# Performance work log

Measured on AMD Instinct MI355X. Metric: run time of the kernel, lower is better.

The kernel has to match this reference:

```python
import jax, jax.numpy as jnp
import numpy as np


def setup_inputs() -> dict:
    key = jax.random.key(0)
    kq, kk, kv = jax.random.split(key, 3)
    B, H, S, D = 4, 16, 2048, 64
    q = jax.random.normal(kq, (B, H, S, D), dtype=jnp.float32)
    k = jax.random.normal(kk, (B, H, S, D), dtype=jnp.float32)
    v = jax.random.normal(kv, (B, H, S, D), dtype=jnp.float32)
    return {"q": q, "k": k, "v": v}


def reference(q, k, v):
    # Flash-attention math (causal=True, softmax_scale = 1/sqrt(head_dim)).
    D = q.shape[-1]
    scale = 1.0 / np.sqrt(D).astype(np.float32)
    # scores: [B, H, Sq, Sk]
    scores = jnp.einsum('bhqd,bhkd->bhqk', q, k) * scale
    Sq, Sk = scores.shape[-2], scores.shape[-1]
    causal_mask = jnp.tril(jnp.ones((Sq, Sk), dtype=bool))  # [Sq, Sk]
    neg_inf = jnp.asarray(jnp.finfo(scores.dtype).min, scores.dtype)
    scores = jnp.where(causal_mask, scores, neg_inf)
    probs = jax.nn.softmax(scores, axis=-1)
    out = jnp.einsum('bhqk,bhkd->bhqd', probs, v)
    return out
```

## Files before the change

kernel.cpp:

```cpp
#include <hip/hip_runtime.h>
#include <hip/hip_bf16.h>

#define S_LEN 2048
#define DH 64
#define QBLK 128
#define KVBLK 64
#define LDPK 72
#define LDPV 68

typedef __attribute__((ext_vector_type(4)))  float f32x4;
typedef __attribute__((ext_vector_type(16))) float f32x16;
typedef __attribute__((ext_vector_type(8)))  short short8v;
typedef __attribute__((ext_vector_type(4)))  unsigned uint4v;
typedef __attribute__((ext_vector_type(2)))  unsigned uint2v;

__device__ __forceinline__ unsigned cvt_pk(float a, float b) {
    unsigned r;
    asm("v_cvt_pk_bf16_f32 %0, %1, %2" : "=v"(r) : "v"(a), "v"(b));
    return r;
}

__global__ __launch_bounds__(512) void fa_fwd_kernel(
    const float* __restrict__ Q, const float* __restrict__ K,
    const float* __restrict__ V, float* __restrict__ O)
{
    const int tid  = threadIdx.x;
    const int lane = tid & 63;
    const int w    = tid >> 6;
    const int bh   = blockIdx.x & 63;
    const int p    = blockIdx.x >> 6;

    const int qb = (w < 4) ? (15 - p) : p;
    const int q0 = qb * QBLK + (w & 3) * 32;
    const int kv_end = (16 - p) * QBLK;

    const size_t base = (size_t)bh * S_LEN * DH;
    const float* Qg = Q + base;
    const float* Kg = K + base;
    const float* Vg = V + base;
    float*       Og = O + base;

    __shared__ __align__(16) short K_lds[2][KVBLK][LDPK];
    __shared__ __align__(16) short V_lds[2][DH][LDPV];

    const int q  = lane & 31;
    const int hi = lane >> 5;
    const int kr = tid >> 3;
    const int dc = (tid & 7) * 8;
    const int vd = tid & 63;
    const int vg = tid >> 6;

    unsigned kpfu[4], vpf[4];

    auto prefetch = [&](int kvb) {
        const float* kp = Kg + (size_t)(kvb + kr) * DH + dc;
        f32x4 a = *(const f32x4*)kp;
        f32x4 b = *(const f32x4*)(kp + 4);
        kpfu[0] = cvt_pk(a[0], a[1]); kpfu[1] = cvt_pk(a[2], a[3]);
        kpfu[2] = cvt_pk(b[0], b[1]); kpfu[3] = cvt_pk(b[2], b[3]);
        #pragma unroll
        for (int i = 0; i < 4; ++i) {
            int kv = vg * 8 + i * 2;
            float x = Vg[(size_t)(kvb + kv) * DH + vd];
            float y = Vg[(size_t)(kvb + kv + 1) * DH + vd];
            vpf[i] = cvt_pk(x, y);
        }
    };

    auto stage = [&](int b) {
        uint4v u = {kpfu[0], kpfu[1], kpfu[2], kpfu[3]};
        *(uint4v*)&K_lds[b][kr][dc] = u;
        #pragma unroll
        for (int i = 0; i < 4; ++i) {
            int kv = vg * 8 + i * 2;
            *(unsigned*)((char*)&V_lds[b][0][0] + vd * (LDPV * 2) + kv * 2) = vpf[i];
        }
    };

    const float qscale = 0.125f * 1.44269504088896340736f;

    short8v qfrag[4];
    #pragma unroll
    for (int ds = 0; ds < 4; ++ds) {
        const float* qp = Qg + (size_t)(q0 + q) * DH + ds * 16 + hi * 8;
        f32x4 a = *(const f32x4*)qp;
        f32x4 b = *(const f32x4*)(qp + 4);
        uint4v u;
        u[0] = cvt_pk(a[0] * qscale, a[1] * qscale);
        u[1] = cvt_pk(a[2] * qscale, a[3] * qscale);
        u[2] = cvt_pk(b[0] * qscale, b[1] * qscale);
        u[3] = cvt_pk(b[2] * qscale, b[3] * qscale);
        qfrag[ds] = __builtin_bit_cast(short8v, u);
    }

    f32x16 o_acc[2];
    o_acc[0] = (f32x16)(0.f);
    o_acc[1] = (f32x16)(0.f);
    float m_run = -1e30f, l_run = 0.f;

    prefetch(0);
    stage(0);
    int cur = 0;
    __syncthreads();

    #pragma unroll 1
    for (int kvb = 0; kvb < kv_end; kvb += KVBLK) {
        int nkv = kvb + KVBLK;
        const bool have = nkv < kv_end;
        if (have) prefetch(nkv);

        if (kvb <= q0) {
            const short (*Kc)[LDPK] = K_lds[cur];
            const char* Vc = (const char*)&V_lds[cur][0][0];

            f32x16 s_acc[2];
            s_acc[0] = (f32x16)(0.f);
            s_acc[1] = (f32x16)(0.f);

            __builtin_amdgcn_s_setprio(1);
            #pragma unroll
            for (int ds = 0; ds < 4; ++ds) {
                #pragma unroll
                for (int kt = 0; kt < 2; ++kt) {
                    short8v kf = *(const short8v*)&Kc[kt * 32 + q][ds * 16 + hi * 8];
                    s_acc[kt] = __builtin_amdgcn_mfma_f32_32x32x16_bf16(
                        kf, qfrag[ds], s_acc[kt], 0, 0, 0);
                }
            }
            __builtin_amdgcn_s_setprio(0);

            const int qrow = q0 + q;
            if (kvb + KVBLK - 1 > q0) {
                #pragma unroll
                for (int kt = 0; kt < 2; ++kt)
                    #pragma unroll
                    for (int r = 0; r < 16; ++r) {
                        int kv = kvb + kt * 32 + (r & 3) + 8 * (r >> 2) + 4 * hi;
                        if (kv > qrow) s_acc[kt][r] = -1e30f;
                    }
            }

            float tl = -1e30f;
            #pragma unroll
            for (int kt = 0; kt < 2; ++kt)
                #pragma unroll
                for (int r = 0; r < 16; ++r)
                    tl = fmaxf(tl, s_acc[kt][r]);
            float tmax = fmaxf(tl, __shfl_xor(tl, 32));

            if (!__all(tmax <= m_run + 8.0f)) {
                float mnew = fmaxf(m_run, tmax);
                float corr = __builtin_amdgcn_exp2f(m_run - mnew);
                m_run = mnew;
                l_run *= corr;
                #pragma unroll
                for (int dt = 0; dt < 2; ++dt)
                    #pragma unroll
                    for (int r = 0; r < 16; ++r)
                        o_acc[dt][r] *= corr;
            }

            float rsum = 0.f;
            #pragma unroll
            for (int kt = 0; kt < 2; ++kt)
                #pragma unroll
                for (int r = 0; r < 16; ++r) {
                    float pe = __builtin_amdgcn_exp2f(s_acc[kt][r] - m_run);
                    s_acc[kt][r] = pe;
                    rsum += pe;
                }
            rsum += __shfl_xor(rsum, 32);
            l_run += rsum;

            unsigned pk_[2][8];
            #pragma unroll
            for (int kt = 0; kt < 2; ++kt)
                #pragma unroll
                for (int m = 0; m < 8; ++m)
                    pk_[kt][m] = cvt_pk(s_acc[kt][2 * m], s_acc[kt][2 * m + 1]);

            __builtin_amdgcn_s_setprio(1);
            #pragma unroll
            for (int s = 0; s < 4; ++s) {
                const int kt = s >> 1, bofs = 4 * (s & 1);
                uint4v bu = {pk_[kt][bofs], pk_[kt][bofs + 1],
                             pk_[kt][bofs + 2], pk_[kt][bofs + 3]};
                short8v pb = __builtin_bit_cast(short8v, bu);
                #pragma unroll
                for (int dt = 0; dt < 2; ++dt) {
                    const char* vrow = Vc + (size_t)(dt * 32 + q) * (LDPV * 2);
                    uint2v lo = *(const uint2v*)(vrow + (16 * s + 4 * hi) * 2);
                    uint2v h2 = *(const uint2v*)(vrow + (16 * s + 8 + 4 * hi) * 2);
                    uint4v au = {lo[0], lo[1], h2[0], h2[1]};
                    short8v va = __builtin_bit_cast(short8v, au);
                    o_acc[dt] = __builtin_amdgcn_mfma_f32_32x32x16_bf16(
                        va, pb, o_acc[dt], 0, 0, 0);
                }
            }
            __builtin_amdgcn_s_setprio(0);
        }

        if (have) {
            stage(cur ^ 1);
            __syncthreads();
        }
        cur ^= 1;
    }

    float inv = 1.0f / l_run;
    float* orow = Og + (size_t)(q0 + q) * DH;
    #pragma unroll
    for (int dt = 0; dt < 2; ++dt) {
        #pragma unroll
        for (int g = 0; g < 4; ++g) {
            f32x4 ov = {o_acc[dt][4 * g] * inv,     o_acc[dt][4 * g + 1] * inv,
                        o_acc[dt][4 * g + 2] * inv, o_acc[dt][4 * g + 3] * inv};
            *(f32x4*)(orow + dt * 32 + 8 * g + 4 * hi) = ov;
        }
    }
}

extern "C" void kernel_launch(void* const* d_in, const int* in_sizes, int n_in,
                              void* d_out, int out_size, void* d_ws, size_t ws_size,
                              hipStream_t stream) {
    const float* q = (const float*)d_in[0];
    const float* k = (const float*)d_in[1];
    const float* v = (const float*)d_in[2];
    float* out = (float*)d_out;
    fa_fwd_kernel<<<dim3(512), dim3(512), 0, stream>>>(q, k, v, out);
}
```

Measured before the change: 65.68 us.

## Double KV tile to 128 rows with split half-tile prefetch and staging

The KV block grows from 64 to 128 rows. Each loop iteration computes two 64-row halves and spreads the global loads and LDS stores for the next block across those halves. This halves the number of block-wide barriers and gives more compute to hide load latency behind. In exchange LDS use roughly doubles and register pressure rises from the second set of prefetch registers.

```diff
diff --git a/kernel.cpp b/kernel.cpp
--- a/kernel.cpp
+++ b/kernel.cpp
@@ -4,9 +4,9 @@
 #define S_LEN 2048
 #define DH 64
 #define QBLK 128
-#define KVBLK 64
+#define KVBLK 128
 #define LDPK 72
-#define LDPV 68
+#define LDPV 132
 
 typedef __attribute__((ext_vector_type(4)))  float f32x4;
 typedef __attribute__((ext_vector_type(16))) float f32x16;
@@ -50,30 +50,52 @@
     const int vd = tid & 63;
     const int vg = tid >> 6;
 
-    unsigned kpfu[4], vpf[4];
-
-    auto prefetch = [&](int kvb) {
+    unsigned kA[4], vA[4], kB[4], vB[4];
+
+    auto prefA = [&](int kvb) {
         const float* kp = Kg + (size_t)(kvb + kr) * DH + dc;
         f32x4 a = *(const f32x4*)kp;
         f32x4 b = *(const f32x4*)(kp + 4);
-        kpfu[0] = cvt_pk(a[0], a[1]); kpfu[1] = cvt_pk(a[2], a[3]);
-        kpfu[2] = cvt_pk(b[0], b[1]); kpfu[3] = cvt_pk(b[2], b[3]);
+        kA[0] = cvt_pk(a[0], a[1]); kA[1] = cvt_pk(a[2], a[3]);
+        kA[2] = cvt_pk(b[0], b[1]); kA[3] = cvt_pk(b[2], b[3]);
         #pragma unroll
         for (int i = 0; i < 4; ++i) {
             int kv = vg * 8 + i * 2;
             float x = Vg[(size_t)(kvb + kv) * DH + vd];
             float y = Vg[(size_t)(kvb + kv + 1) * DH + vd];
-            vpf[i] = cvt_pk(x, y);
-        }
-    };
-
-    auto stage = [&](int b) {
-        uint4v u = {kpfu[0], kpfu[1], kpfu[2], kpfu[3]};
+            vA[i] = cvt_pk(x, y);
+        }
+    };
+    auto prefB = [&](int kvb) {
+        const float* kp = Kg + (size_t)(kvb + kr) * DH + dc;
+        f32x4 a = *(const f32x4*)kp;
+        f32x4 b = *(const f32x4*)(kp + 4);
+        kB[0] = cvt_pk(a[0], a[1]); kB[1] = cvt_pk(a[2], a[3]);
+        kB[2] = cvt_pk(b[0], b[1]); kB[3] = cvt_pk(b[2], b[3]);
+        #pragma unroll
+        for (int i = 0; i < 4; ++i) {
+            int kv = vg * 8 + i * 2;
+            float x = Vg[(size_t)(kvb + kv) * DH + vd];
+            float y = Vg[(size_t)(kvb + kv + 1) * DH + vd];
+            vB[i] = cvt_pk(x, y);
+        }
+    };
+    auto stageA = [&](int b) {
+        uint4v u = {kA[0], kA[1], kA[2], kA[3]};
         *(uint4v*)&K_lds[b][kr][dc] = u;
         #pragma unroll
         for (int i = 0; i < 4; ++i) {
             int kv = vg * 8 + i * 2;
-            *(unsigned*)((char*)&V_lds[b][0][0] + vd * (LDPV * 2) + kv * 2) = vpf[i];
+            *(unsigned*)((char*)&V_lds[b][0][0] + vd * (LDPV * 2) + kv * 2) = vA[i];
+        }
+    };
+    auto stageB = [&](int b) {
+        uint4v u = {kB[0], kB[1], kB[2], kB[3]};
+        *(uint4v*)&K_lds[b][64 + kr][dc] = u;
+        #pragma unroll
+        for (int i = 0; i < 4; ++i) {
+            int kv = 64 + vg * 8 + i * 2;
+            *(unsigned*)((char*)&V_lds[b][0][0] + vd * (LDPV * 2) + kv * 2) = vB[i];
         }
     };
 
@@ -98,110 +120,118 @@
     o_acc[1] = (f32x16)(0.f);
     float m_run = -1e30f, l_run = 0.f;
 
-    prefetch(0);
-    stage(0);
-    int cur = 0;
-    __syncthreads();
-
-    #pragma unroll 1
-    for (int kvb = 0; kvb < kv_end; kvb += KVBLK) {
-        int nkv = kvb + KVBLK;
-        const bool have = nkv < kv_end;
-        if (have) prefetch(nkv);
-
-        if (kvb <= q0) {
-            const short (*Kc)[LDPK] = K_lds[cur];
-            const char* Vc = (const char*)&V_lds[cur][0][0];
-
-            f32x16 s_acc[2];
-            s_acc[0] = (f32x16)(0.f);
-            s_acc[1] = (f32x16)(0.f);
-
-            __builtin_amdgcn_s_setprio(1);
-            #pragma unroll
-            for (int ds = 0; ds < 4; ++ds) {
-                #pragma unroll
-                for (int kt = 0; kt < 2; ++kt) {
-                    short8v kf = *(const short8v*)&Kc[kt * 32 + q][ds * 16 + hi * 8];
-                    s_acc[kt] = __builtin_amdgcn_mfma_f32_32x32x16_bf16(
-                        kf, qfrag[ds], s_acc[kt], 0, 0, 0);
-                }
+    auto compute64 = [&](int cur, int kvb_eff, int h) {
+        const short (*Kc)[LDPK] = K_lds[cur];
+        const char* Vc = (const char*)&V_lds[cur][0][0];
+
+        f32x16 s_acc[2];
+        s_acc[0] = (f32x16)(0.f);
+        s_acc[1] = (f32x16)(0.f);
+
+        __builtin_amdgcn_s_setprio(1);
+        #pragma unroll
+        for (int ds = 0; ds < 4; ++ds) {
+            #pragma unroll
+            for (int kt = 0; kt < 2; ++kt) {
+                short8v kf = *(const short8v*)&Kc[h + kt * 32 + q][ds * 16 + hi * 8];
+                s_acc[kt] = __builtin_amdgcn_mfma_f32_32x32x16_bf16(
+                    kf, qfrag[ds], s_acc[kt], 0, 0, 0);
             }
-            __builtin_amdgcn_s_setprio(0);
-
-            const int qrow = q0 + q;
-            if (kvb + KVBLK - 1 > q0) {
-                #pragma unroll
-                for (int kt = 0; kt < 2; ++kt)
-                    #pragma unroll
-                    for (int r = 0; r < 16; ++r) {
-                        int kv = kvb + kt * 32 + (r & 3) + 8 * (r >> 2) + 4 * hi;
-                        if (kv > qrow) s_acc[kt][r] = -1e30f;
-                    }
-            }
-
-            float tl = -1e30f;
-            #pragma unroll
-            for (int kt = 0; kt < 2; ++kt)
-                #pragma unroll
-                for (int r = 0; r < 16; ++r)
-                    tl = fmaxf(tl, s_acc[kt][r]);
-            float tmax = fmaxf(tl, __shfl_xor(tl, 32));
-
-            if (!__all(tmax <= m_run + 8.0f)) {
-                float mnew = fmaxf(m_run, tmax);
-                float corr = __builtin_amdgcn_exp2f(m_run - mnew);
-                m_run = mnew;
-                l_run *= corr;
-                #pragma unroll
-                for (int dt = 0; dt < 2; ++dt)
-                    #pragma unroll
-                    for (int r = 0; r < 16; ++r)
-                        o_acc[dt][r] *= corr;
-            }
-
-            float rsum = 0.f;
+        }
+        __builtin_amdgcn_s_setprio(0);
+
+        const int qrow = q0 + q;
+        if (kvb_eff + 63 > q0) {
             #pragma unroll
             for (int kt = 0; kt < 2; ++kt)
                 #pragma unroll
                 for (int r = 0; r < 16; ++r) {
-                    float pe = __builtin_amdgcn_exp2f(s_acc[kt][r] - m_run);
-                    s_acc[kt][r] = pe;
-                    rsum += pe;
+                    int kv = kvb_eff + kt * 32 + (r & 3) + 8 * (r >> 2) + 4 * hi;
+                    if (kv > qrow) s_acc[kt][r] = -1e30f;
                 }
-            rsum += __shfl_xor(rsum, 32);
-            l_run += rsum;
-
-            unsigned pk_[2][8];
-            #pragma unroll
-            for (int kt = 0; kt < 2; ++kt)
+        }
+
+        float tl = -1e30f;
+        #pragma unroll
+        for (int kt = 0; kt < 2; ++kt)
+            #pragma unroll
+            for (int r = 0; r < 16; ++r)
+                tl = fmaxf(tl, s_acc[kt][r]);
+        float tmax = fmaxf(tl, __shfl_xor(tl, 32));
+
+        if (!__all(tmax <= m_run + 8.0f)) {
+            float mnew = fmaxf(m_run, tmax);
+            float corr = __builtin_amdgcn_exp2f(m_run - mnew);
+            m_run = mnew;
+            l_run *= corr;
+            #pragma unroll
+            for (int dt = 0; dt < 2; ++dt)
                 #pragma unroll
-                for (int m = 0; m < 8; ++m)
-                    pk_[kt][m] = cvt_pk(s_acc[kt][2 * m], s_acc[kt][2 * m + 1]);
-
-            __builtin_amdgcn_s_setprio(1);
-            #pragma unroll
-            for (int s = 0; s < 4; ++s) {
-                const int kt = s >> 1, bofs = 4 * (s & 1);
-                uint4v bu = {pk_[kt][bofs], pk_[kt][bofs + 1],
-                             pk_[kt][bofs + 2], pk_[kt][bofs + 3]};
-                short8v pb = __builtin_bit_cast(short8v, bu);
-                #pragma unroll
-                for (int dt = 0; dt < 2; ++dt) {
-                    const char* vrow = Vc + (size_t)(dt * 32 + q) * (LDPV * 2);
-                    uint2v lo = *(const uint2v*)(vrow + (16 * s + 4 * hi) * 2);
-                    uint2v h2 = *(const uint2v*)(vrow + (16 * s + 8 + 4 * hi) * 2);
-                    uint4v au = {lo[0], lo[1], h2[0], h2[1]};
-                    short8v va = __builtin_bit_cast(short8v, au);
-                    o_acc[dt] = __builtin_amdgcn_mfma_f32_32x32x16_bf16(
-                        va, pb, o_acc[dt], 0, 0, 0);
-                }
+                for (int r = 0; r < 16; ++r)
+                    o_acc[dt][r] *= corr;
+        }
+
+        float rsum = 0.f;
+        #pragma unroll
+        for (int kt = 0; kt < 2; ++kt)
+            #pragma unroll
+            for (int r = 0; r < 16; ++r) {
+                float pe = __builtin_amdgcn_exp2f(s_acc[kt][r] - m_run);
+                s_acc[kt][r] = pe;
+                rsum += pe;
             }
-            __builtin_amdgcn_s_setprio(0);
-        }
-
+        rsum += __shfl_xor(rsum, 32);
+        l_run += rsum;
+
+        unsigned pk_[2][8];
+        #pragma unroll
+        for (int kt = 0; kt < 2; ++kt)
+            #pragma unroll
+            for (int m = 0; m < 8; ++m)
+                pk_[kt][m] = cvt_pk(s_acc[kt][2 * m], s_acc[kt][2 * m + 1]);
+
+        __builtin_amdgcn_s_setprio(1);
+        #pragma unroll
+        for (int ss = 0; ss < 4; ++ss) {
+            const int kt = ss >> 1, bofs = 4 * (ss & 1);
+            uint4v bu = {pk_[kt][bofs], pk_[kt][bofs + 1],
+                         pk_[kt][bofs + 2], pk_[kt][bofs + 3]};
+            short8v pb = __builtin_bit_cast(short8v, bu);
+            #pragma unroll
+            for (int dt = 0; dt < 2; ++dt) {
+                const char* vrow = Vc + (size_t)(dt * 32 + q) * (LDPV * 2);
+                uint2v lo = *(const uint2v*)(vrow + (h + 16 * ss + 4 * hi) * 2);
+                uint2v h2 = *(const uint2v*)(vrow + (h + 16 * ss + 8 + 4 * hi) * 2);
+                uint4v au = {lo[0], lo[1], h2[0], h2[1]};
+                short8v va = __builtin_bit_cast(short8v, au);
+                o_acc[dt] = __builtin_amdgcn_mfma_f32_32x32x16_bf16(
+                    va, pb, o_acc[dt], 0, 0, 0);
+            }
+        }
+        __builtin_amdgcn_s_setprio(0);
+    };
+
+    prefA(0);
+    prefB(64);
+    stageA(0);
+    stageB(0);
+    int cur = 0;
+    __syncthreads();
+
+    #pragma unroll 1
+    for (int kvb = 0; kvb < kv_end; kvb += KVBLK) {
+        const int nkv = kvb + KVBLK;
+        const bool have = nkv < kv_end;
+
+        if (have) prefA(nkv);
+        if (kvb <= q0) compute64(cur, kvb, 0);
         if (have) {
-            stage(cur ^ 1);
+            prefB(nkv + 64);
+            stageA(cur ^ 1);
+        }
+        if (kvb + 64 <= q0) compute64(cur, kvb + 64, 64);
+        if (have) {
+            stageB(cur ^ 1);
             __syncthreads();
         }
         cur ^= 1;
```

Result: slower. 84.44 us (+28.6%).

## Split KV range across wave halves with LDS merge of partial softmax states

Applied to the files above, without the earlier changes.

Instead of each half of the workgroup owning a different query block, both halves now process the same 128-row query block. Each half covers half of its KV range, and the two query blocks of a pair run one after another. The partial max, sum and output accumulators are merged through LDS at the end. This balances causal work between waves and is meant to cut the time waves sit idle on masked tiles. In exchange it adds extra barriers per iteration, drops the double buffering (each half now uses its own single buffer with two syncs), and adds an LDS reduction epilogue.

```diff
diff --git a/kernel.cpp b/kernel.cpp
--- a/kernel.cpp
+++ b/kernel.cpp
@@ -3,8 +3,6 @@
 
 #define S_LEN 2048
 #define DH 64
-#define QBLK 128
-#define KVBLK 64
 #define LDPK 72
 #define LDPV 68
 
@@ -30,9 +28,8 @@
     const int bh   = blockIdx.x & 63;
     const int p    = blockIdx.x >> 6;
 
-    const int qb = (w < 4) ? (15 - p) : p;
-    const int q0 = qb * QBLK + (w & 3) * 32;
-    const int kv_end = (16 - p) * QBLK;
+    const int half = w >> 2;
+    const int rt   = w & 3;
 
     const size_t base = (size_t)bh * S_LEN * DH;
     const float* Qg = Q + base;
@@ -40,8 +37,10 @@
     const float* Vg = V + base;
     float*       Og = O + base;
 
-    __shared__ __align__(16) short K_lds[2][KVBLK][LDPK];
-    __shared__ __align__(16) short V_lds[2][DH][LDPV];
+    __shared__ __align__(16) char smem[35840];
+    short (*K_lds)[64][LDPK] = (short(*)[64][LDPK])smem;
+    short (*V_lds)[64][LDPV] = (short(*)[64][LDPV])(smem + 18432);
+    float (*Mbuf)[64][34]    = (float(*)[64][34])smem;
 
     const int q  = lane & 31;
     const int hi = lane >> 5;
@@ -50,173 +49,207 @@
     const int vd = tid & 63;
     const int vg = tid >> 6;
 
-    unsigned kpfu[4], vpf[4];
-
-    auto prefetch = [&](int kvb) {
-        const float* kp = Kg + (size_t)(kvb + kr) * DH + dc;
-        f32x4 a = *(const f32x4*)kp;
-        f32x4 b = *(const f32x4*)(kp + 4);
-        kpfu[0] = cvt_pk(a[0], a[1]); kpfu[1] = cvt_pk(a[2], a[3]);
-        kpfu[2] = cvt_pk(b[0], b[1]); kpfu[3] = cvt_pk(b[2], b[3]);
+    unsigned kpf[2][4], vpf[2][4];
+
+    auto prefetch = [&](int kvbL, int kvbH) {
         #pragma unroll
-        for (int i = 0; i < 4; ++i) {
-            int kv = vg * 8 + i * 2;
-            float x = Vg[(size_t)(kvb + kv) * DH + vd];
-            float y = Vg[(size_t)(kvb + kv + 1) * DH + vd];
-            vpf[i] = cvt_pk(x, y);
+        for (int hh = 0; hh < 2; ++hh) {
+            const int kvb = hh ? kvbH : kvbL;
+            const float* kp = Kg + (size_t)(kvb + kr) * DH + dc;
+            f32x4 a = *(const f32x4*)kp;
+            f32x4 b = *(const f32x4*)(kp + 4);
+            kpf[hh][0] = cvt_pk(a[0], a[1]); kpf[hh][1] = cvt_pk(a[2], a[3]);
+            kpf[hh][2] = cvt_pk(b[0], b[1]); kpf[hh][3] = cvt_pk(b[2], b[3]);
+            #pragma unroll
+            for (int i = 0; i < 4; ++i) {
+                int kv = vg * 8 + i * 2;
+                float x = Vg[(size_t)(kvb + kv) * DH + vd];
+                float y = Vg[(size_t)(kvb + kv + 1) * DH + vd];
+                vpf[hh][i] = cvt_pk(x, y);
+            }
         }
     };
 
-    auto stage = [&](int b) {
-        uint4v u = {kpfu[0], kpfu[1], kpfu[2], kpfu[3]};
-        *(uint4v*)&K_lds[b][kr][dc] = u;
+    auto stage = [&]() {
         #pragma unroll
-        for (int i = 0; i < 4; ++i) {
-            int kv = vg * 8 + i * 2;
-            *(unsigned*)((char*)&V_lds[b][0][0] + vd * (LDPV * 2) + kv * 2) = vpf[i];
+        for (int hh = 0; hh < 2; ++hh) {
+            uint4v u = {kpf[hh][0], kpf[hh][1], kpf[hh][2], kpf[hh][3]};
+            *(uint4v*)&K_lds[hh][kr][dc] = u;
+            #pragma unroll
+            for (int i = 0; i < 4; ++i) {
+                int kv = vg * 8 + i * 2;
+                *(unsigned*)((char*)&V_lds[hh][0][0] + vd * (LDPV * 2) + kv * 2) = vpf[hh][i];
+            }
         }
     };
 
     const float qscale = 0.125f * 1.44269504088896340736f;
 
-    short8v qfrag[4];
-    #pragma unroll
-    for (int ds = 0; ds < 4; ++ds) {
-        const float* qp = Qg + (size_t)(q0 + q) * DH + ds * 16 + hi * 8;
-        f32x4 a = *(const f32x4*)qp;
-        f32x4 b = *(const f32x4*)(qp + 4);
-        uint4v u;
-        u[0] = cvt_pk(a[0] * qscale, a[1] * qscale);
-        u[1] = cvt_pk(a[2] * qscale, a[3] * qscale);
-        u[2] = cvt_pk(b[0] * qscale, b[1] * qscale);
-        u[3] = cvt_pk(b[2] * qscale, b[3] * qscale);
-        qfrag[ds] = __builtin_bit_cast(short8v, u);
-    }
-
-    f32x16 o_acc[2];
-    o_acc[0] = (f32x16)(0.f);
-    o_acc[1] = (f32x16)(0.f);
-    float m_run = -1e30f, l_run = 0.f;
-
-    prefetch(0);
-    stage(0);
-    int cur = 0;
-    __syncthreads();
-
     #pragma unroll 1
-    for (int kvb = 0; kvb < kv_end; kvb += KVBLK) {
-        int nkv = kvb + KVBLK;
-        const bool have = nkv < kv_end;
-        if (have) prefetch(nkv);
-
-        if (kvb <= q0) {
-            const short (*Kc)[LDPK] = K_lds[cur];
-            const char* Vc = (const char*)&V_lds[cur][0][0];
-
-            f32x16 s_acc[2];
-            s_acc[0] = (f32x16)(0.f);
-            s_acc[1] = (f32x16)(0.f);
-
-            __builtin_amdgcn_s_setprio(1);
-            #pragma unroll
-            for (int ds = 0; ds < 4; ++ds) {
-                #pragma unroll
-                for (int kt = 0; kt < 2; ++kt) {
-                    short8v kf = *(const short8v*)&Kc[kt * 32 + q][ds * 16 + hi * 8];
-                    s_acc[kt] = __builtin_amdgcn_mfma_f32_32x32x16_bf16(
-                        kf, qfrag[ds], s_acc[kt], 0, 0, 0);
-                }
-            }
-            __builtin_amdgcn_s_setprio(0);
-
-            const int qrow = q0 + q;
-            if (kvb + KVBLK - 1 > q0) {
+    for (int t = 0; t < 2; ++t) {
+        const int qb = (t == 0) ? (15 - p) : p;
+        const int nT = qb + 1;
+        const int Hb = nT * 64;
+        const int q0 = qb * 128 + rt * 32;
+
+        short8v qfrag[4];
+        #pragma unroll
+        for (int ds = 0; ds < 4; ++ds) {
+            const float* qp = Qg + (size_t)(q0 + q) * DH + ds * 16 + hi * 8;
+            f32x4 a = *(const f32x4*)qp;
+            f32x4 b = *(const f32x4*)(qp + 4);
+            uint4v u;
+            u[0] = cvt_pk(a[0] * qscale, a[1] * qscale);
+            u[1] = cvt_pk(a[2] * qscale, a[3] * qscale);
+            u[2] = cvt_pk(b[0] * qscale, b[1] * qscale);
+            u[3] = cvt_pk(b[2] * qscale, b[3] * qscale);
+            qfrag[ds] = __builtin_bit_cast(short8v, u);
+        }
+
+        f32x16 o_acc[2];
+        o_acc[0] = (f32x16)(0.f);
+        o_acc[1] = (f32x16)(0.f);
+        float m_run = -1e30f, l_run = 0.f;
+
+        prefetch(0, Hb);
+        stage();
+        __syncthreads();
+
+        #pragma unroll 1
+        for (int s = 0; s < nT; ++s) {
+            const bool have = (s + 1) < nT;
+            if (have) prefetch((s + 1) * 64, Hb + (s + 1) * 64);
+
+            const int kvb_eff = half ? (Hb + s * 64) : (s * 64);
+            if (kvb_eff <= q0) {
+                const short (*Kc)[LDPK] = K_lds[half];
+                const char* Vc = (const char*)&V_lds[half][0][0];
+
+                f32x16 s_acc[2];
+                s_acc[0] = (f32x16)(0.f);
+                s_acc[1] = (f32x16)(0.f);
+
+                __builtin_amdgcn_s_setprio(1);
+                #pragma unroll
+                for (int ds = 0; ds < 4; ++ds) {
+                    #pragma unroll
+                    for (int kt = 0; kt < 2; ++kt) {
+                        short8v kf = *(const short8v*)&Kc[kt * 32 + q][ds * 16 + hi * 8];
+                        s_acc[kt] = __builtin_amdgcn_mfma_f32_32x32x16_bf16(
+                            kf, qfrag[ds], s_acc[kt], 0, 0, 0);
+                    }
+                }
+                __builtin_amdgcn_s_setprio(0);
+
+                const int qrow = q0 + q;
+                if (kvb_eff + 63 > q0) {
+                    #pragma unroll
+                    for (int kt = 0; kt < 2; ++kt)
+                        #pragma unroll
+                        for (int r = 0; r < 16; ++r) {
+                            int kv = kvb_eff + kt * 32 + (r & 3) + 8 * (r >> 2) + 4 * hi;
+                            if (kv > qrow) s_acc[kt][r] = -1e30f;
+                        }
+                }
+
+                float tl = -1e30f;
                 #pragma unroll
                 for (int kt = 0; kt < 2; ++kt)
                     #pragma unroll
+                    for (int r = 0; r < 16; ++r)
+                        tl = fmaxf(tl, s_acc[kt][r]);
+                float tmax = fmaxf(tl, __shfl_xor(tl, 32));
+
+                if (!__all(tmax <= m_run + 8.0f)) {
+                    float mnew = fmaxf(m_run, tmax);
+                    float corr = __builtin_amdgcn_exp2f(m_run - mnew);
+                    m_run = mnew;
+                    l_run *= corr;
+                    #pragma unroll
+                    for (int dt = 0; dt < 2; ++dt)
+                        #pragma unroll
+                        for (int r = 0; r < 16; ++r)
+                            o_acc[dt][r] *= corr;
+                }
+
+                float rsum = 0.f;
+                #pragma unroll
+                for (int kt = 0; kt < 2; ++kt)
+                    #pragma unroll
                     for (int r = 0; r < 16; ++r) {
-                        int kv = kvb + kt * 32 + (r & 3) + 8 * (r >> 2) + 4 * hi;
-                        if (kv > qrow) s_acc[kt][r] = -1e30f;
+                        float pe = __builtin_amdgcn_exp2f(s_acc[kt][r] - m_run);
+                        s_acc[kt][r] = pe;
+                        rsum += pe;
                     }
-            }
-
-            float tl = -1e30f;
-            #pragma unroll
-            for (int kt = 0; kt < 2; ++kt)
+                rsum += __shfl_xor(rsum, 32);
+                l_run += rsum;
+
+                unsigned pk_[2][8];
+                #pragma unroll
+                for (int kt = 0; kt < 2; ++kt)
+                    #pragma unroll
+                    for (int m = 0; m < 8; ++m)
+                        pk_[kt][m] = cvt_pk(s_acc[kt][2 * m], s_acc[kt][2 * m + 1]);
+
+                __builtin_amdgcn_s_setprio(1);
+                #pragma unroll
+                for (int ss = 0; ss < 4; ++ss) {
+                    const int kt = ss >> 1, bofs = 4 * (ss & 1);
+                    uint4v bu = {pk_[kt][bofs], pk_[kt][bofs + 1],
+                                 pk_[kt][bofs + 2], pk_[kt][bofs + 3]};
+                    short8v pb = __builtin_bit_cast(short8v, bu);
+                    #pragma unroll
+                    for (int dt = 0; dt < 2; ++dt) {
+                        const char* vrow = Vc + (size_t)(dt * 32 + q) * (LDPV * 2);
+                        uint2v lo = *(const uint2v*)(vrow + (16 * ss + 4 * hi) * 2);
+                        uint2v h2 = *(const uint2v*)(vrow + (16 * ss + 8 + 4 * hi) * 2);
+                        uint4v au = {lo[0], lo[1], h2[0], h2[1]};
+                        short8v va = __builtin_bit_cast(short8v, au);
+                        o_acc[dt] = __builtin_amdgcn_mfma_f32_32x32x16_bf16(
+                            va, pb, o_acc[dt], 0, 0, 0);
+                    }
+                }
+                __builtin_amdgcn_s_setprio(0);
+            }
+
+            __syncthreads();
+            if (have) stage();
+            __syncthreads();
+        }
+
+        if (half == 1) {
+            float* mb = Mbuf[rt][lane];
+            mb[0] = m_run;
+            mb[1] = l_run;
+            #pragma unroll
+            for (int d2 = 0; d2 < 2; ++d2)
                 #pragma unroll
                 for (int r = 0; r < 16; ++r)
-                    tl = fmaxf(tl, s_acc[kt][r]);
-            float tmax = fmaxf(tl, __shfl_xor(tl, 32));
-
-            if (!__all(tmax <= m_run + 8.0f)) {
-                float mnew = fmaxf(m_run, tmax);
-                float corr = __builtin_amdgcn_exp2f(m_run - mnew);
-                m_run = mnew;
-                l_run *= corr;
-                #pragma unroll
-                for (int dt = 0; dt < 2; ++dt)
-                    #pragma unroll
-                    for (int r = 0; r < 16; ++r)
-                        o_acc[dt][r] *= corr;
-            }
-
-            float rsum = 0.f;
-            #pragma unroll
-            for (int kt = 0; kt < 2; ++kt)
-                #pragma unroll
-                for (int r = 0; r < 16; ++r) {
-                    float pe = __builtin_amdgcn_exp2f(s_acc[kt][r] - m_run);
-                    s_acc[kt][r] = pe;
-                    rsum += pe;
-                }
-            rsum += __shfl_xor(rsum, 32);
-            l_run += rsum;
-
-            unsigned pk_[2][8];
-            #pragma unroll
-            for (int kt = 0; kt < 2; ++kt)
-                #pragma unroll
-                for (int m = 0; m < 8; ++m)
-                    pk_[kt][m] = cvt_pk(s_acc[kt][2 * m], s_acc[kt][2 * m + 1]);
-
-            __builtin_amdgcn_s_setprio(1);
-            #pragma unroll
-            for (int s = 0; s < 4; ++s) {
-                const int kt = s >> 1, bofs = 4 * (s & 1);
-                uint4v bu = {pk_[kt][bofs], pk_[kt][bofs + 1],
-                             pk_[kt][bofs + 2], pk_[kt][bofs + 3]};
-                short8v pb = __builtin_bit_cast(short8v, bu);
-                #pragma unroll
-                for (int dt = 0; dt < 2; ++dt) {
-                    const char* vrow = Vc + (size_t)(dt * 32 + q) * (LDPV * 2);
-                    uint2v lo = *(const uint2v*)(vrow + (16 * s + 4 * hi) * 2);
-                    uint2v h2 = *(const uint2v*)(vrow + (16 * s + 8 + 4 * hi) * 2);
-                    uint4v au = {lo[0], lo[1], h2[0], h2[1]};
-                    short8v va = __builtin_bit_cast(short8v, au);
-                    o_acc[dt] = __builtin_amdgcn_mfma_f32_32x32x16_bf16(
-                        va, pb, o_acc[dt], 0, 0, 0);
-                }
-            }
-            __builtin_amdgcn_s_setprio(0);
-        }
-
-        if (have) {
-            stage(cur ^ 1);
-            __syncthreads();
-        }
-        cur ^= 1;
-    }
-
-    float inv = 1.0f / l_run;
-    float* orow = Og + (size_t)(q0 + q) * DH;
-    #pragma unroll
-    for (int dt = 0; dt < 2; ++dt) {
-        #pragma unroll
-        for (int g = 0; g < 4; ++g) {
-            f32x4 ov = {o_acc[dt][4 * g] * inv,     o_acc[dt][4 * g + 1] * inv,
-                        o_acc[dt][4 * g + 2] * inv, o_acc[dt][4 * g + 3] * inv};
-            *(f32x4*)(orow + dt * 32 + 8 * g + 4 * hi) = ov;
-        }
+                    mb[2 + d2 * 16 + r] = o_acc[d2][r];
+        }
+        __syncthreads();
+        if (half == 0) {
+            const float* mb = Mbuf[rt][lane];
+            float mB = mb[0], lB = mb[1];
+            float mN = fmaxf(m_run, mB);
+            float sA = __builtin_amdgcn_exp2f(m_run - mN);
+            float sB = __builtin_amdgcn_exp2f(mB - mN);
+            float inv = 1.0f / (l_run * sA + lB * sB);
+            float* orow = Og + (size_t)(q0 + q) * DH;
+            #pragma unroll
+            for (int dt = 0; dt < 2; ++dt) {
+                #pragma unroll
+                for (int g = 0; g < 4; ++g) {
+                    f32x4 ov;
+                    #pragma unroll
+                    for (int i2 = 0; i2 < 4; ++i2)
+                        ov[i2] = (o_acc[dt][4 * g + i2] * sA +
+                                  mb[2 + dt * 16 + 4 * g + i2] * sB) * inv;
+                    *(f32x4*)(orow + dt * 32 + 8 * g + 4 * hi) = ov;
+                }
+            }
+        }
+        __syncthreads();
     }
 }
 
```

Result: slower. 93.33 us (+42.1%).

## Deepen K/V global prefetch to two tiles ahead with A/B register sets

Applied to the files above, without the earlier changes.

Global K/V loads are now issued two KV tiles ahead, alternating between two raw fp32 register sets, and the bf16 conversion moves to LDS staging time. The loop is unrolled by two so each compute tile overlaps with loads for a tile further in the future. This is meant to hide more global memory latency, at the cost of extra registers holding unconverted fp32 data, which may pressure occupancy at 512 threads.

```diff
diff --git a/kernel.cpp b/kernel.cpp
--- a/kernel.cpp
+++ b/kernel.cpp
@@ -33,6 +33,7 @@
     const int qb = (w < 4) ? (15 - p) : p;
     const int q0 = qb * QBLK + (w & 3) * 32;
     const int kv_end = (16 - p) * QBLK;
+    const int T = kv_end >> 6;
 
     const size_t base = (size_t)bh * S_LEN * DH;
     const float* Qg = Q + base;
@@ -50,30 +51,51 @@
     const int vd = tid & 63;
     const int vg = tid >> 6;
 
-    unsigned kpfu[4], vpf[4];
-
-    auto prefetch = [&](int kvb) {
+    f32x4 kA0, kA1, kB0, kB1;
+    float vA[8], vB[8];
+
+    auto issueA = [&](int kvb) {
         const float* kp = Kg + (size_t)(kvb + kr) * DH + dc;
-        f32x4 a = *(const f32x4*)kp;
-        f32x4 b = *(const f32x4*)(kp + 4);
-        kpfu[0] = cvt_pk(a[0], a[1]); kpfu[1] = cvt_pk(a[2], a[3]);
-        kpfu[2] = cvt_pk(b[0], b[1]); kpfu[3] = cvt_pk(b[2], b[3]);
-        #pragma unroll
-        for (int i = 0; i < 4; ++i) {
-            int kv = vg * 8 + i * 2;
-            float x = Vg[(size_t)(kvb + kv) * DH + vd];
-            float y = Vg[(size_t)(kvb + kv + 1) * DH + vd];
-            vpf[i] = cvt_pk(x, y);
-        }
-    };
-
-    auto stage = [&](int b) {
-        uint4v u = {kpfu[0], kpfu[1], kpfu[2], kpfu[3]};
+        kA0 = *(const f32x4*)kp;
+        kA1 = *(const f32x4*)(kp + 4);
+        #pragma unroll
+        for (int i = 0; i < 4; ++i) {
+            int kv = vg * 8 + i * 2;
+            vA[2 * i]     = Vg[(size_t)(kvb + kv) * DH + vd];
+            vA[2 * i + 1] = Vg[(size_t)(kvb + kv + 1) * DH + vd];
+        }
+    };
+    auto issueB = [&](int kvb) {
+        const float* kp = Kg + (size_t)(kvb + kr) * DH + dc;
+        kB0 = *(const f32x4*)kp;
+        kB1 = *(const f32x4*)(kp + 4);
+        #pragma unroll
+        for (int i = 0; i < 4; ++i) {
+            int kv = vg * 8 + i * 2;
+            vB[2 * i]     = Vg[(size_t)(kvb + kv) * DH + vd];
+            vB[2 * i + 1] = Vg[(size_t)(kvb + kv + 1) * DH + vd];
+        }
+    };
+    auto stageA = [&](int b) {
+        uint4v u = {cvt_pk(kA0[0], kA0[1]), cvt_pk(kA0[2], kA0[3]),
+                    cvt_pk(kA1[0], kA1[1]), cvt_pk(kA1[2], kA1[3])};
         *(uint4v*)&K_lds[b][kr][dc] = u;
         #pragma unroll
         for (int i = 0; i < 4; ++i) {
             int kv = vg * 8 + i * 2;
-            *(unsigned*)((char*)&V_lds[b][0][0] + vd * (LDPV * 2) + kv * 2) = vpf[i];
+            *(unsigned*)((char*)&V_lds[b][0][0] + vd * (LDPV * 2) + kv * 2) =
+                cvt_pk(vA[2 * i], vA[2 * i + 1]);
+        }
+    };
+    auto stageB = [&](int b) {
+        uint4v u = {cvt_pk(kB0[0], kB0[1]), cvt_pk(kB0[2], kB0[3]),
+                    cvt_pk(kB1[0], kB1[1]), cvt_pk(kB1[2], kB1[3])};
+        *(uint4v*)&K_lds[b][kr][dc] = u;
+        #pragma unroll
+        for (int i = 0; i < 4; ++i) {
+            int kv = vg * 8 + i * 2;
+            *(unsigned*)((char*)&V_lds[b][0][0] + vd * (LDPV * 2) + kv * 2) =
+                cvt_pk(vB[2 * i], vB[2 * i + 1]);
         }
     };
 
@@ -98,110 +120,117 @@
     o_acc[1] = (f32x16)(0.f);
     float m_run = -1e30f, l_run = 0.f;
 
-    prefetch(0);
-    stage(0);
-    int cur = 0;
-    __syncthreads();
-
-    #pragma unroll 1
-    for (int kvb = 0; kvb < kv_end; kvb += KVBLK) {
-        int nkv = kvb + KVBLK;
-        const bool have = nkv < kv_end;
-        if (have) prefetch(nkv);
-
-        if (kvb <= q0) {
-            const short (*Kc)[LDPK] = K_lds[cur];
-            const char* Vc = (const char*)&V_lds[cur][0][0];
-
-            f32x16 s_acc[2];
-            s_acc[0] = (f32x16)(0.f);
-            s_acc[1] = (f32x16)(0.f);
-
-            __builtin_amdgcn_s_setprio(1);
-            #pragma unroll
-            for (int ds = 0; ds < 4; ++ds) {
-                #pragma unroll
-                for (int kt = 0; kt < 2; ++kt) {
-                    short8v kf = *(const short8v*)&Kc[kt * 32 + q][ds * 16 + hi * 8];
-                    s_acc[kt] = __builtin_amdgcn_mfma_f32_32x32x16_bf16(
-                        kf, qfrag[ds], s_acc[kt], 0, 0, 0);
-                }
+    auto computeTile = [&](int cur, int kvb) {
+        const short (*Kc)[LDPK] = K_lds[cur];
+        const char* Vc = (const char*)&V_lds[cur][0][0];
+
+        f32x16 s_acc[2];
+        s_acc[0] = (f32x16)(0.f);
+        s_acc[1] = (f32x16)(0.f);
+
+        __builtin_amdgcn_s_setprio(1);
+        #pragma unroll
+        for (int ds = 0; ds < 4; ++ds) {
+            #pragma unroll
+            for (int kt = 0; kt < 2; ++kt) {
+                short8v kf = *(const short8v*)&Kc[kt * 32 + q][ds * 16 + hi * 8];
+                s_acc[kt] = __builtin_amdgcn_mfma_f32_32x32x16_bf16(
+                    kf, qfrag[ds], s_acc[kt], 0, 0, 0);
             }
-            __builtin_amdgcn_s_setprio(0);
-
-            const int qrow = q0 + q;
-            if (kvb + KVBLK - 1 > q0) {
-                #pragma unroll
-                for (int kt = 0; kt < 2; ++kt)
-                    #pragma unroll
-                    for (int r = 0; r < 16; ++r) {
-                        int kv = kvb + kt * 32 + (r & 3) + 8 * (r >> 2) + 4 * hi;
-                        if (kv > qrow) s_acc[kt][r] = -1e30f;
-                    }
-            }
-
-            float tl = -1e30f;
-            #pragma unroll
-            for (int kt = 0; kt < 2; ++kt)
-                #pragma unroll
-                for (int r = 0; r < 16; ++r)
-                    tl = fmaxf(tl, s_acc[kt][r]);
-            float tmax = fmaxf(tl, __shfl_xor(tl, 32));
-
-            if (!__all(tmax <= m_run + 8.0f)) {
-                float mnew = fmaxf(m_run, tmax);
-                float corr = __builtin_amdgcn_exp2f(m_run - mnew);
-                m_run = mnew;
-                l_run *= corr;
-                #pragma unroll
-                for (int dt = 0; dt < 2; ++dt)
-                    #pragma unroll
-                    for (int r = 0; r < 16; ++r)
-                        o_acc[dt][r] *= corr;
-            }
-
-            float rsum = 0.f;
+        }
+        __builtin_amdgcn_s_setprio(0);
+
+        const int qrow = q0 + q;
+        if (kvb + KVBLK - 1 > q0) {
             #pragma unroll
             for (int kt = 0; kt < 2; ++kt)
                 #pragma unroll
                 for (int r = 0; r < 16; ++r) {
-                    float pe = __builtin_amdgcn_exp2f(s_acc[kt][r] - m_run);
-                    s_acc[kt][r] = pe;
-                    rsum += pe;
+                    int kv = kvb + kt * 32 + (r & 3) + 8 * (r >> 2) + 4 * hi;
+                    if (kv > qrow) s_acc[kt][r] = -1e30f;
                 }
-            rsum += __shfl_xor(rsum, 32);
-            l_run += rsum;
-
-            unsigned pk_[2][8];
-            #pragma unroll
-            for (int kt = 0; kt < 2; ++kt)
+        }
+
+        float tl = -1e30f;
+        #pragma unroll
+        for (int kt = 0; kt < 2; ++kt)
+            #pragma unroll
+            for (int r = 0; r < 16; ++r)
+                tl = fmaxf(tl, s_acc[kt][r]);
+        float tmax = fmaxf(tl, __shfl_xor(tl, 32));
+
+        if (!__all(tmax <= m_run + 8.0f)) {
+            float mnew = fmaxf(m_run, tmax);
+            float corr = __builtin_amdgcn_exp2f(m_run - mnew);
+            m_run = mnew;
+            l_run *= corr;
+            #pragma unroll
+            for (int dt = 0; dt < 2; ++dt)
                 #pragma unroll
-                for (int m = 0; m < 8; ++m)
-                    pk_[kt][m] = cvt_pk(s_acc[kt][2 * m], s_acc[kt][2 * m + 1]);
-
-            __builtin_amdgcn_s_setprio(1);
-            #pragma unroll
-            for (int s = 0; s < 4; ++s) {
-                const int kt = s >> 1, bofs = 4 * (s & 1);
-                uint4v bu = {pk_[kt][bofs], pk_[kt][bofs + 1],
-                             pk_[kt][bofs + 2], pk_[kt][bofs + 3]};
-                short8v pb = __builtin_bit_cast(short8v, bu);
-                #pragma unroll
-                for (int dt = 0; dt < 2; ++dt) {
-                    const char* vrow = Vc + (size_t)(dt * 32 + q) * (LDPV * 2);
-                    uint2v lo = *(const uint2v*)(vrow + (16 * s + 4 * hi) * 2);
-                    uint2v h2 = *(const uint2v*)(vrow + (16 * s + 8 + 4 * hi) * 2);
-                    uint4v au = {lo[0], lo[1], h2[0], h2[1]};
-                    short8v va = __builtin_bit_cast(short8v, au);
-                    o_acc[dt] = __builtin_amdgcn_mfma_f32_32x32x16_bf16(
-                        va, pb, o_acc[dt], 0, 0, 0);
-                }
+                for (int r = 0; r < 16; ++r)
+                    o_acc[dt][r] *= corr;
+        }
+
+        float rsum = 0.f;
+        #pragma unroll
+        for (int kt = 0; kt < 2; ++kt)
+            #pragma unroll
+            for (int r = 0; r < 16; ++r) {
+                float pe = __builtin_amdgcn_exp2f(s_acc[kt][r] - m_run);
+                s_acc[kt][r] = pe;
+                rsum += pe;
             }
-            __builtin_amdgcn_s_setprio(0);
-        }
-
-        if (have) {
-            stage(cur ^ 1);
+        rsum += __shfl_xor(rsum, 32);
+        l_run += rsum;
+
+        unsigned pk_[2][8];
+        #pragma unroll
+        for (int kt = 0; kt < 2; ++kt)
+            #pragma unroll
+            for (int m = 0; m < 8; ++m)
+                pk_[kt][m] = cvt_pk(s_acc[kt][2 * m], s_acc[kt][2 * m + 1]);
+
+        __builtin_amdgcn_s_setprio(1);
+        #pragma unroll
+        for (int ss = 0; ss < 4; ++ss) {
+            const int kt = ss >> 1, bofs = 4 * (ss & 1);
+            uint4v bu = {pk_[kt][bofs], pk_[kt][bofs + 1],
+                         pk_[kt][bofs + 2], pk_[kt][bofs + 3]};
+            short8v pb = __builtin_bit_cast(short8v, bu);
+            #pragma unroll
+            for (int dt = 0; dt < 2; ++dt) {
+                const char* vrow = Vc + (size_t)(dt * 32 + q) * (LDPV * 2);
+                uint2v lo = *(const uint2v*)(vrow + (16 * ss + 4 * hi) * 2);
+                uint2v h2 = *(const uint2v*)(vrow + (16 * ss + 8 + 4 * hi) * 2);
+                uint4v au = {lo[0], lo[1], h2[0], h2[1]};
+                short8v va = __builtin_bit_cast(short8v, au);
+                o_acc[dt] = __builtin_amdgcn_mfma_f32_32x32x16_bf16(
+                    va, pb, o_acc[dt], 0, 0, 0);
+            }
+        }
+        __builtin_amdgcn_s_setprio(0);
+    };
+
+    issueA(0);
+    if (T > 1) issueB(64);
+    stageA(0);
+    int cur = 0;
+    __syncthreads();
+
+    #pragma unroll 1
+    for (int s = 0; s < T; s += 2) {
+        if (s + 2 < T) issueA((s + 2) * 64);
+        if (s * 64 <= q0) computeTile(cur, s * 64);
+        if (s + 1 < T) {
+            stageB(cur ^ 1);
+            __syncthreads();
+        }
+        cur ^= 1;
+
+        if (s + 3 < T) issueB((s + 3) * 64);
+        if ((s + 1) * 64 <= q0) computeTile(cur, (s + 1) * 64);
+        if (s + 2 < T) {
+            stageA(cur ^ 1);
             __syncthreads();
         }
         cur ^= 1;
```

Measured after the change: 81.25 us. 1.24x slower.
